# Optimization experiments

Measured on AMD Instinct MI355X. Metric: run time of the kernel, lower is better.

The kernel has to match this reference:

```python
import jax, jax.numpy as jnp
import numpy as np
from jax.scipy.special import logsumexp

VOCAB, NLABEL, NSTATE = 32000, 16, 64
BATCH, MAXLEN = 512, 512


def setup_inputs() -> dict:
    key = jax.random.key(0)
    k1, k2, k3, k4, k5 = jax.random.split(key, 5)
    sentences = jax.random.randint(k1, (BATCH, MAXLEN), 0, VOCAB)
    length = jax.random.randint(k2, (BATCH,), 1, MAXLEN + 1)  # valid lengths in [1, MAXLEN]
    # parameters, uniform(-0.5, 0.5) as in reset_parameter()
    emb = jax.random.uniform(k3, (VOCAB, NSTATE), minval=-0.5, maxval=0.5, dtype=jnp.float32)
    transition = jax.random.uniform(k4, (NSTATE, NSTATE), minval=-0.5, maxval=0.5, dtype=jnp.float32)
    output = jax.random.uniform(k5, (NLABEL, NSTATE), minval=-0.5, maxval=0.5, dtype=jnp.float32)
    return {"sentences": sentences, "length": length, "emb": emb,
            "transition": transition, "output": output}


def reference(sentences, length, emb, transition, output):
    batch = sentences.shape[0]
    # emission log-probs per timestep: [T, B, S]
    emission = jax.nn.log_softmax(emb[sentences.T], axis=-1)
    trans = jax.nn.log_softmax(transition, axis=-1)  # [S, S]

    def step(f, e):
        # log-space matrix-vector product: logsumexp over previous state
        nf = logsumexp(trans[None, :, :] + f[:, None, :], axis=-1) + e  # [B, S]
        return nf, nf

    f0 = emission[0]
    _, rest = jax.lax.scan(step, f0, emission[1:])
    forwards = jnp.concatenate([f0[None], rest], axis=0)  # [T, B, S]
    hidden = forwards[length - 1, jnp.arange(batch)]  # [B, S]
    out_log = jax.nn.log_softmax(output, axis=-1)  # [L, S]
    score = logsumexp(out_log[None, :, :] + hidden[:, None, :], axis=-1)  # [B, L]
    return score
```

## Files before the change

### kernel.cpp

```cpp
#include <hip/hip_runtime.h>
#include <stdint.h>

#define VOCAB  32000
#define NSTATE 64
#define NLABEL 16
#define BATCH  512
#define MAXLEN 512
#define CHUNK  64
#define NC     (MAXLEN / CHUNK)

#define LOG2E 1.44269504088896340736f
#define LN2_D 0.69314718055994530942

typedef float  f32x4  __attribute__((ext_vector_type(4)));
typedef short  bf16x8 __attribute__((ext_vector_type(8)));
typedef float  v2f    __attribute__((ext_vector_type(2)));

#if defined(__has_builtin) && __has_builtin(__builtin_amdgcn_exp2f)
#define EXP2(x) __builtin_amdgcn_exp2f(x)
#else
#define EXP2(x) exp2f(x)
#endif
#if defined(__has_builtin) && __has_builtin(__builtin_amdgcn_logf)
#define LOG2(x) __builtin_amdgcn_logf(x)
#else
#define LOG2(x) log2f(x)
#endif

__device__ __forceinline__ float wave_max64(float x) {
#pragma unroll
  for (int off = 32; off > 0; off >>= 1) x = fmaxf(x, __shfl_xor(x, off, 64));
  return x;
}
__device__ __forceinline__ float wave_sum64(float x) {
#pragma unroll
  for (int off = 32; off > 0; off >>= 1) x += __shfl_xor(x, off, 64);
  return x;
}
__device__ __forceinline__ float bcast0(float x) {
  return __uint_as_float(__builtin_amdgcn_readfirstlane(__float_as_uint(x)));
}
__device__ __forceinline__ double shfl_xor_d(double x, int off) {
  union { double d; int i[2]; } u;
  u.d = x;
  u.i[0] = __shfl_xor(u.i[0], off, 64);
  u.i[1] = __shfl_xor(u.i[1], off, 64);
  return u.d;
}
__device__ __forceinline__ unsigned short f2bf(float x) {
  uint32_t u = __float_as_uint(x);
  return (unsigned short)((u + 0x7FFFu + ((u >> 16) & 1u)) >> 16);
}
__device__ __forceinline__ float bf2f(unsigned short h) {
  return __uint_as_float(((uint32_t)h) << 16);
}
__device__ __forceinline__ int swz(int a) { return a ^ (((a >> 7) & 7) << 4); }

__global__ void prep_emb_k(const float* __restrict__ emb, float* __restrict__ emb2) {
  const int w = blockIdx.x * 4 + (threadIdx.x >> 6);
  const int s = threadIdx.x & 63;
  const float v = emb[w * NSTATE + s] * LOG2E;
  const float m = wave_max64(v);
  const float ss = wave_sum64(EXP2(v - m));
  emb2[w * NSTATE + s] = v - m - LOG2(ss);
}

__global__ void prep_mats_k(const float* __restrict__ trans, const float* __restrict__ outp,
                            float* __restrict__ W, float* __restrict__ out2) {
  const int r = blockIdx.x, s = threadIdx.x;
  if (r < NSTATE) {
    const float v = trans[r * NSTATE + s] * LOG2E;
    const float m = wave_max64(v);
    const float ss = wave_sum64(EXP2(v - m));
    W[r * NSTATE + s] = EXP2(v - m - LOG2(ss));
  } else {
    const int l = r - NSTATE;
    const float v = outp[l * NSTATE + s] * LOG2E;
    const float m = wave_max64(v);
    const float ss = wave_sum64(EXP2(v - m));
    out2[l * NSTATE + s] = v - m - LOG2(ss);
  }
}

__global__ void prep_wfrag_k(const float* __restrict__ W, bf16x8* __restrict__ Wb) {
  const int l = threadIdx.x;
  const int l15 = l & 15, lh = l >> 4;
#pragma unroll
  for (int mi = 0; mi < 4; ++mi)
#pragma unroll
    for (int ks = 0; ks < 2; ++ks) {
      bf16x8 v;
#pragma unroll
      for (int i = 0; i < 8; ++i)
        v[i] = (short)f2bf(W[(mi * 16 + l15) * 64 + ks * 32 + 8 * lh + i]);
      Wb[(mi * 2 + ks) * 64 + l] = v;
    }
}

__global__ void prep_musum2_k(const int* __restrict__ sents, const float* __restrict__ emb2,
                              const int* __restrict__ length, double* __restrict__ musum) {
  const int b = blockIdx.x;
  const int l = threadIdx.x;
  const int len = length[b];
  double acc = 0.0;
#pragma unroll
  for (int k = 0; k < 8; ++k) {
    const int t = k * 64 + l;
    const int id = sents[b * MAXLEN + t];
    const float e0 = emb2[id * NSTATE];
    if (t < len) acc += (double)e0;
  }
#pragma unroll
  for (int off = 32; off > 0; off >>= 1) acc += shfl_xor_d(acc, off);
  if (l == 0) musum[b] = acc;
}

__global__ __launch_bounds__(64, 2) void phaseA_k(
    const int* __restrict__ sents, const int* __restrict__ length,
    const float* __restrict__ emb2, const bf16x8* __restrict__ Wb,
    unsigned short* __restrict__ Mout, int* __restrict__ Mexp) {
  const int tid = blockIdx.x;
  const int b = tid >> 3;
  const int c = tid & 7;
  const int l = threadIdx.x;
  const int l15 = l & 15, lh = l >> 4;

  __shared__ __align__(16) unsigned short MT[4096];
  __shared__ __align__(16) float q_lds[NSTATE];
  __shared__ __align__(16) int ids[CHUNK];

  ids[l] = sents[b * MAXLEN + c * CHUNK + l];

  bf16x8 wf[4][2];
#pragma unroll
  for (int mi = 0; mi < 4; ++mi)
#pragma unroll
    for (int ks = 0; ks < 2; ++ks)
      wf[mi][ks] = Wb[(mi * 2 + ks) * 64 + l];

  {
    const int4 z{0, 0, 0, 0};
#pragma unroll
    for (int k = 0; k < 8; ++k)
      *reinterpret_cast<int4*>(reinterpret_cast<char*>(MT) + k * 1024 + l * 16) = z;
    const int dbyte = swz(128 * l + 2 * l);
    *reinterpret_cast<unsigned short*>(reinterpret_cast<char*>(MT) + dbyte) = 0x3F80u;
  }

  const int len = length[b];
  const int t0 = c * CHUNK;
  const int start = (c == 0) ? 1 : t0;
  const int end_ = ((len - 1) < (t0 + CHUNK - 1)) ? (len - 1) : (t0 + CHUNK - 1);
  const int K = end_ - start + 1;
  int MUc = 0;

  if (K > 0) {
    int idx = start - t0;
    int idc = ids[idx];
    float e_cur = emb2[idc * NSTATE + l];
    float rnorm = 1.0f;
    bool rn_pending = false;

    for (int j = 0; j < K; ++j) {
      const int idxn = (j + 1 < K) ? (idx + 1) : idx;
      const int idn = ids[idxn];
      const float e_nxt = emb2[idn * NSTATE + l];

      const float se = bcast0(e_cur);
      q_lds[l] = EXP2(e_cur - se);

      float samp = 0.f;
#pragma unroll
      for (int pass = 0; pass < 2; ++pass) {
        bf16x8 mf[2][2];
#pragma unroll
        for (int ks = 0; ks < 2; ++ks)
#pragma unroll
          for (int nn = 0; nn < 2; ++nn) {
            const int n = (pass * 2 + nn) * 16 + l15;
            const int byte = swz(128 * n + 64 * ks + 16 * lh);
            mf[ks][nn] = *reinterpret_cast<const bf16x8*>(
                reinterpret_cast<const char*>(MT) + byte);
          }
#pragma unroll
        for (int mi = 0; mi < 4; ++mi) {
          f32x4 qf = *reinterpret_cast<const f32x4*>(q_lds + mi * 16 + 4 * lh);
          if (rn_pending) qf *= rnorm;
#pragma unroll
          for (int nn = 0; nn < 2; ++nn) {
            f32x4 acc{0.f, 0.f, 0.f, 0.f};
            acc = __builtin_amdgcn_mfma_f32_16x16x32_bf16(wf[mi][0], mf[0][nn], acc, 0, 0, 0);
            acc = __builtin_amdgcn_mfma_f32_16x16x32_bf16(wf[mi][1], mf[1][nn], acc, 0, 0, 0);
            acc *= qf;
            if (pass == 0 && nn == 0 && mi == 0) samp = acc.x;
            const uint32_t lo = (uint32_t)f2bf(acc.x) | ((uint32_t)f2bf(acc.y) << 16);
            const uint32_t hi = (uint32_t)f2bf(acc.z) | ((uint32_t)f2bf(acc.w) << 16);
            const int n = (pass * 2 + nn) * 16 + l15;
            const int wbyte = swz(128 * n + 2 * (mi * 16 + 4 * lh));
            *reinterpret_cast<uint2*>(reinterpret_cast<char*>(MT) + wbyte) = uint2{lo, hi};
          }
        }
      }
      rn_pending = false;
      if (((j & 7) == 7) && (j + 1 < K)) {
        const uint32_t u = __builtin_amdgcn_readfirstlane(__float_as_uint(samp));
        const int ex = (int)((u >> 23) & 255u) - 127;
        rnorm = __uint_as_float((uint32_t)(127 - ex) << 23);
        rn_pending = true;
        MUc += ex;
      }
      e_cur = e_nxt;
      idx = idxn;
    }
  }

  unsigned short* dst = Mout + (size_t)tid * 4096;
#pragma unroll
  for (int k = 0; k < 8; ++k) {
    const int4 v = *reinterpret_cast<const int4*>(
        reinterpret_cast<const char*>(MT) + k * 1024 + l * 16);
    *reinterpret_cast<int4*>(reinterpret_cast<char*>(dst) + k * 1024 + l * 16) = v;
  }
  if (l == 0) Mexp[tid] = MUc;
}

__global__ __launch_bounds__(64) void phaseB_k(
    const int* __restrict__ sents, const int* __restrict__ length,
    const float* __restrict__ emb2, const float* __restrict__ out2,
    const unsigned short* __restrict__ Mout, const int* __restrict__ Mexp,
    const double* __restrict__ musum, float* __restrict__ score) {
  const int b = blockIdx.x;
  const int l = threadIdx.x;
  const int len = length[b];

  const int id0 = sents[b * MAXLEN];
  const float e0 = emb2[id0 * NSTATE + l];
  const float se0 = bcast0(e0);
  float p = EXP2(e0 - se0);
  int MUi = 0;

  for (int c = 0; c < NC && c * CHUNK < len; ++c) {
    const unsigned short* M = Mout + ((size_t)(b * NC + c)) * 4096;
    float acc = 0.f;
#pragma unroll 8
    for (int n = 0; n < 64; ++n) {
      const float pn = __shfl(p, n, 64);
      const int byte = swz(128 * n + 2 * l);
      const unsigned short h = *reinterpret_cast<const unsigned short*>(
          reinterpret_cast<const char*>(M) + byte);
      acc = fmaf(bf2f(h), pn, acc);
    }
    p = acc;
    MUi += Mexp[b * NC + c];
    const uint32_t u = __builtin_amdgcn_readfirstlane(__float_as_uint(p));
    const int ex = (int)((u >> 23) & 255u) - 127;
    p *= __uint_as_float((uint32_t)(127 - ex) << 23);
    MUi += ex;
  }

  const float f = LOG2(p);
  const double base = musum[b] + (double)MUi;
  for (int ll = 0; ll < NLABEL; ++ll) {
    const float y = out2[ll * NSTATE + l] + f;
    const float m = wave_max64(y);
    const float ssum = wave_sum64(EXP2(y - m));
    if (l == 0)
      score[b * NLABEL + ll] = (float)((base + (double)m + (double)LOG2(ssum)) * LN2_D);
  }
}

__global__ __launch_bounds__(64, 1) void iohmm_fwd_fb(
    const int* __restrict__ sents, const int* __restrict__ length,
    const float* __restrict__ emb, const float* __restrict__ trans,
    const float* __restrict__ outp, float* __restrict__ score) {
  const int b = blockIdx.x;
  const int s = threadIdx.x;
  __shared__ __align__(16) float p_lds[2][NSTATE];
  v2f w2[NSTATE / 2];
  {
    float wr[NSTATE];
#pragma unroll
    for (int j = 0; j < 16; ++j) {
      const float4 q = *reinterpret_cast<const float4*>(trans + s * NSTATE + 4 * j);
      wr[4 * j + 0] = q.x * LOG2E; wr[4 * j + 1] = q.y * LOG2E;
      wr[4 * j + 2] = q.z * LOG2E; wr[4 * j + 3] = q.w * LOG2E;
    }
    float m = -1e30f;
#pragma unroll
    for (int j = 0; j < NSTATE; ++j) m = fmaxf(m, wr[j]);
    float ss = 0.f;
#pragma unroll
    for (int j = 0; j < NSTATE; ++j) ss += EXP2(wr[j] - m);
    const float d = m + LOG2(ss);
#pragma unroll
    for (int j = 0; j < NSTATE / 2; ++j)
      w2[j] = v2f{EXP2(wr[2 * j] - d), EXP2(wr[2 * j + 1] - d)};
  }
  const int len = length[b];
  auto EMIT = [&](int t) -> float {
    const int tc = t < MAXLEN ? t : MAXLEN - 1;
    return emb[sents[b * MAXLEN + tc] * NSTATE + s] * LOG2E;
  };
  float e0 = EMIT(0);
  {
    const float dm = wave_max64(e0);
    const float dsum = wave_sum64(EXP2(e0 - dm));
    e0 = e0 - dm - LOG2(dsum);
  }
  const float se0 = bcast0(e0);
  float p = EXP2(e0 - se0);
  double MU = (double)se0;
  int MUi = 0;
  for (int t = 1; t < len; ++t) {
    float* pb = p_lds[t & 1];
    pb[s] = p;
    __builtin_amdgcn_sched_barrier(0);
    const float eR = EMIT(t);
    const float4* pb4 = reinterpret_cast<const float4*>(pb);
    v2f A0{0.f, 0.f}, A1 = A0, A2 = A0, A3 = A0;
#pragma unroll
    for (int j = 0; j < 8; ++j) {
      const float4 qa = pb4[2 * j + 0];
      const float4 qb = pb4[2 * j + 1];
      A0 = __builtin_elementwise_fma(w2[4 * j + 0], v2f{qa.x, qa.y}, A0);
      A1 = __builtin_elementwise_fma(w2[4 * j + 1], v2f{qa.z, qa.w}, A1);
      A2 = __builtin_elementwise_fma(w2[4 * j + 2], v2f{qb.x, qb.y}, A2);
      A3 = __builtin_elementwise_fma(w2[4 * j + 3], v2f{qb.z, qb.w}, A3);
    }
    const v2f S0 = A0 + A2, S1 = A1 + A3;
    const v2f U = S0 + S1;
    const float sum = U.x + U.y;
    const float dm = wave_max64(eR);
    const float dsum = wave_sum64(EXP2(eR - dm));
    const float e = eR - dm - LOG2(dsum);
    const float se = bcast0(e);
    p = sum * EXP2(e - se);
    if ((t & 15) == 0) {
      const uint32_t u = __builtin_amdgcn_readfirstlane(__float_as_uint(p));
      const int ex = (int)((u >> 23) & 255u) - 127;
      p *= __uint_as_float((uint32_t)(127 - ex) << 23);
      MUi += ex;
    }
    MU += (double)se;
  }
  const float f = LOG2(p);
  const double MUt = MU + (double)MUi;
  for (int ll = 0; ll < NLABEL; ++ll) {
    const float v = outp[ll * NSTATE + s] * LOG2E;
    const float lm = wave_max64(v);
    const float lsum = wave_sum64(EXP2(v - lm));
    const float y = v - lm - LOG2(lsum) + f;
    const float m = wave_max64(y);
    const float ssum = wave_sum64(EXP2(y - m));
    if (s == 0)
      score[b * NLABEL + ll] = (float)((MUt + (double)m + (double)LOG2(ssum)) * LN2_D);
  }
}

extern "C" void kernel_launch(void* const* d_in, const int* in_sizes, int n_in,
                              void* d_out, int out_size, void* d_ws, size_t ws_size,
                              hipStream_t stream) {
  const int* sents = (const int*)d_in[0];
  const int* length = (const int*)d_in[1];
  const float* emb = (const float*)d_in[2];
  const float* trans = (const float*)d_in[3];
  const float* outp = (const float*)d_in[4];
  float* score = (float*)d_out;

  const size_t emb2_off = 0;
  const size_t emb2_sz = (size_t)VOCAB * NSTATE * sizeof(float);
  const size_t W_off = emb2_off + emb2_sz;
  const size_t W_sz = NSTATE * NSTATE * sizeof(float);
  const size_t out2_off = W_off + W_sz;
  const size_t out2_sz = NLABEL * NSTATE * sizeof(float);
  const size_t Wb_off = out2_off + out2_sz;
  const size_t Wb_sz = 8 * 64 * 16;
  const size_t musum_off = Wb_off + Wb_sz;
  const size_t musum_sz = BATCH * sizeof(double);
  const size_t Mexp_off = musum_off + musum_sz;
  const size_t Mexp_sz = (size_t)BATCH * NC * sizeof(int);
  const size_t Mout_off = Mexp_off + Mexp_sz;
  const size_t Mout_sz = (size_t)BATCH * NC * 4096 * sizeof(unsigned short);
  const size_t need = Mout_off + Mout_sz;

  if (ws_size >= need) {
    float* emb2 = (float*)((char*)d_ws + emb2_off);
    float* W = (float*)((char*)d_ws + W_off);
    float* out2 = (float*)((char*)d_ws + out2_off);
    bf16x8* Wb = (bf16x8*)((char*)d_ws + Wb_off);
    double* musum = (double*)((char*)d_ws + musum_off);
    int* Mexp = (int*)((char*)d_ws + Mexp_off);
    unsigned short* Mout = (unsigned short*)((char*)d_ws + Mout_off);

    prep_emb_k<<<VOCAB / 4, 256, 0, stream>>>(emb, emb2);
    prep_mats_k<<<NSTATE + NLABEL, 64, 0, stream>>>(trans, outp, W, out2);
    prep_wfrag_k<<<1, 64, 0, stream>>>(W, Wb);
    prep_musum2_k<<<BATCH, 64, 0, stream>>>(sents, emb2, length, musum);
    phaseA_k<<<BATCH * NC, 64, 0, stream>>>(sents, length, emb2, Wb, Mout, Mexp);
    phaseB_k<<<BATCH, 64, 0, stream>>>(sents, length, emb2, out2, Mout, Mexp, musum, score);
  } else {
    iohmm_fwd_fb<<<BATCH, 64, 0, stream>>>(sents, length, emb, trans, outp, score);
  }
}
```

Before: 304.4 us.

## Fold prep kernels into phase kernels and pack four chunk waves per block

```diff
diff --git a/kernel.cpp b/kernel.cpp
--- a/kernel.cpp
+++ b/kernel.cpp
@@ -1,4 +1,5 @@
 #include <hip/hip_runtime.h>
+#include <hip/hip_bf16.h>
 #include <stdint.h>
 
 #define VOCAB  32000
@@ -47,9 +48,12 @@
   u.i[1] = __shfl_xor(u.i[1], off, 64);
   return u.d;
 }
-__device__ __forceinline__ unsigned short f2bf(float x) {
-  uint32_t u = __float_as_uint(x);
-  return (unsigned short)((u + 0x7FFFu + ((u >> 16) & 1u)) >> 16);
+__device__ __forceinline__ short bfs(float x) {
+  __hip_bfloat16 h = __float2bfloat16(x);
+  return *reinterpret_cast<short*>(&h);
+}
+__device__ __forceinline__ uint32_t pkbf(float lo, float hi) {
+  return (uint32_t)(unsigned short)bfs(lo) | ((uint32_t)(unsigned short)bfs(hi) << 16);
 }
 __device__ __forceinline__ float bf2f(unsigned short h) {
   return __uint_as_float(((uint32_t)h) << 16);
@@ -82,69 +86,42 @@
   }
 }
 
-__global__ void prep_wfrag_k(const float* __restrict__ W, bf16x8* __restrict__ Wb) {
-  const int l = threadIdx.x;
-  const int l15 = l & 15, lh = l >> 4;
-#pragma unroll
-  for (int mi = 0; mi < 4; ++mi)
-#pragma unroll
-    for (int ks = 0; ks < 2; ++ks) {
-      bf16x8 v;
-#pragma unroll
-      for (int i = 0; i < 8; ++i)
-        v[i] = (short)f2bf(W[(mi * 16 + l15) * 64 + ks * 32 + 8 * lh + i]);
-      Wb[(mi * 2 + ks) * 64 + l] = v;
-    }
-}
-
-__global__ void prep_musum2_k(const int* __restrict__ sents, const float* __restrict__ emb2,
-                              const int* __restrict__ length, double* __restrict__ musum) {
-  const int b = blockIdx.x;
-  const int l = threadIdx.x;
-  const int len = length[b];
-  double acc = 0.0;
-#pragma unroll
-  for (int k = 0; k < 8; ++k) {
-    const int t = k * 64 + l;
-    const int id = sents[b * MAXLEN + t];
-    const float e0 = emb2[id * NSTATE];
-    if (t < len) acc += (double)e0;
-  }
-#pragma unroll
-  for (int off = 32; off > 0; off >>= 1) acc += shfl_xor_d(acc, off);
-  if (l == 0) musum[b] = acc;
-}
-
-__global__ __launch_bounds__(64, 2) void phaseA_k(
+__global__ __launch_bounds__(256, 4) void phaseA_k(
     const int* __restrict__ sents, const int* __restrict__ length,
-    const float* __restrict__ emb2, const bf16x8* __restrict__ Wb,
+    const float* __restrict__ emb2, const float* __restrict__ W,
     unsigned short* __restrict__ Mout, int* __restrict__ Mexp) {
-  const int tid = blockIdx.x;
+  const int wid = threadIdx.x >> 6;
+  const int l = threadIdx.x & 63;
+  const int tid = blockIdx.x * 4 + wid;
   const int b = tid >> 3;
   const int c = tid & 7;
-  const int l = threadIdx.x;
   const int l15 = l & 15, lh = l >> 4;
 
-  __shared__ __align__(16) unsigned short MT[4096];
-  __shared__ __align__(16) float q_lds[NSTATE];
-  __shared__ __align__(16) int ids[CHUNK];
-
-  ids[l] = sents[b * MAXLEN + c * CHUNK + l];
+  __shared__ __align__(16) unsigned short MTall[4][4096];
+  char* MTc = reinterpret_cast<char*>(MTall[wid]);
+
+  const int myid = sents[b * MAXLEN + c * CHUNK + l];
 
   bf16x8 wf[4][2];
 #pragma unroll
   for (int mi = 0; mi < 4; ++mi)
 #pragma unroll
-    for (int ks = 0; ks < 2; ++ks)
-      wf[mi][ks] = Wb[(mi * 2 + ks) * 64 + l];
+    for (int ks = 0; ks < 2; ++ks) {
+      const float* wp = W + (mi * 16 + l15) * 64 + ks * 32 + 8 * lh;
+      const float4 a = *reinterpret_cast<const float4*>(wp);
+      const float4 d = *reinterpret_cast<const float4*>(wp + 4);
+      bf16x8 v;
+      v[0] = bfs(a.x); v[1] = bfs(a.y); v[2] = bfs(a.z); v[3] = bfs(a.w);
+      v[4] = bfs(d.x); v[5] = bfs(d.y); v[6] = bfs(d.z); v[7] = bfs(d.w);
+      wf[mi][ks] = v;
+    }
 
   {
     const int4 z{0, 0, 0, 0};
 #pragma unroll
     for (int k = 0; k < 8; ++k)
-      *reinterpret_cast<int4*>(reinterpret_cast<char*>(MT) + k * 1024 + l * 16) = z;
-    const int dbyte = swz(128 * l + 2 * l);
-    *reinterpret_cast<unsigned short*>(reinterpret_cast<char*>(MT) + dbyte) = 0x3F80u;
+      *reinterpret_cast<int4*>(MTc + k * 1024 + l * 16) = z;
+    *reinterpret_cast<unsigned short*>(MTc + swz(130 * l)) = 0x3F80u;
   }
 
   const int len = length[b];
@@ -155,19 +132,28 @@
   int MUc = 0;
 
   if (K > 0) {
-    int idx = start - t0;
-    int idc = ids[idx];
-    float e_cur = emb2[idc * NSTATE + l];
+    const int lastj = end_ - t0;
+    const int j0 = start - t0;
+    float eA = emb2[(size_t)__shfl(myid, j0, 64) * 64 + l];
+    const int j1 = (j0 + 1 <= lastj) ? j0 + 1 : lastj;
+    float eB = emb2[(size_t)__shfl(myid, j1, 64) * 64 + l];
     float rnorm = 1.0f;
-    bool rn_pending = false;
+    bool rnp = false;
 
     for (int j = 0; j < K; ++j) {
-      const int idxn = (j + 1 < K) ? (idx + 1) : idx;
-      const int idn = ids[idxn];
-      const float e_nxt = emb2[idn * NSTATE + l];
-
-      const float se = bcast0(e_cur);
-      q_lds[l] = EXP2(e_cur - se);
+      int jn = j0 + j + 2; jn = (jn <= lastj) ? jn : lastj;
+      const float eC = emb2[(size_t)__shfl(myid, jn, 64) * 64 + l];
+
+      const float se = bcast0(eA);
+      float qv = EXP2(eA - se);
+      if (rnp) qv *= rnorm;
+
+      float qsc[4][4];
+#pragma unroll
+      for (int mi = 0; mi < 4; ++mi)
+#pragma unroll
+        for (int r = 0; r < 4; ++r)
+          qsc[mi][r] = __shfl(qv, mi * 16 + 4 * lh + r, 64);
 
       float samp = 0.f;
 #pragma unroll
@@ -178,47 +164,43 @@
 #pragma unroll
           for (int nn = 0; nn < 2; ++nn) {
             const int n = (pass * 2 + nn) * 16 + l15;
-            const int byte = swz(128 * n + 64 * ks + 16 * lh);
             mf[ks][nn] = *reinterpret_cast<const bf16x8*>(
-                reinterpret_cast<const char*>(MT) + byte);
+                MTc + swz(128 * n + 64 * ks + 16 * lh));
           }
 #pragma unroll
         for (int mi = 0; mi < 4; ++mi) {
-          f32x4 qf = *reinterpret_cast<const f32x4*>(q_lds + mi * 16 + 4 * lh);
-          if (rn_pending) qf *= rnorm;
 #pragma unroll
           for (int nn = 0; nn < 2; ++nn) {
             f32x4 acc{0.f, 0.f, 0.f, 0.f};
             acc = __builtin_amdgcn_mfma_f32_16x16x32_bf16(wf[mi][0], mf[0][nn], acc, 0, 0, 0);
             acc = __builtin_amdgcn_mfma_f32_16x16x32_bf16(wf[mi][1], mf[1][nn], acc, 0, 0, 0);
-            acc *= qf;
+            acc.x *= qsc[mi][0]; acc.y *= qsc[mi][1];
+            acc.z *= qsc[mi][2]; acc.w *= qsc[mi][3];
             if (pass == 0 && nn == 0 && mi == 0) samp = acc.x;
-            const uint32_t lo = (uint32_t)f2bf(acc.x) | ((uint32_t)f2bf(acc.y) << 16);
-            const uint32_t hi = (uint32_t)f2bf(acc.z) | ((uint32_t)f2bf(acc.w) << 16);
+            const uint32_t lo = pkbf(acc.x, acc.y);
+            const uint32_t hi = pkbf(acc.z, acc.w);
             const int n = (pass * 2 + nn) * 16 + l15;
-            const int wbyte = swz(128 * n + 2 * (mi * 16 + 4 * lh));
-            *reinterpret_cast<uint2*>(reinterpret_cast<char*>(MT) + wbyte) = uint2{lo, hi};
+            *reinterpret_cast<uint2*>(MTc + swz(128 * n + 32 * mi + 8 * lh)) =
+                uint2{lo, hi};
           }
         }
       }
-      rn_pending = false;
+      rnp = false;
       if (((j & 7) == 7) && (j + 1 < K)) {
         const uint32_t u = __builtin_amdgcn_readfirstlane(__float_as_uint(samp));
         const int ex = (int)((u >> 23) & 255u) - 127;
         rnorm = __uint_as_float((uint32_t)(127 - ex) << 23);
-        rn_pending = true;
+        rnp = true;
         MUc += ex;
       }
-      e_cur = e_nxt;
-      idx = idxn;
+      eA = eB; eB = eC;
     }
   }
 
   unsigned short* dst = Mout + (size_t)tid * 4096;
 #pragma unroll
   for (int k = 0; k < 8; ++k) {
-    const int4 v = *reinterpret_cast<const int4*>(
-        reinterpret_cast<const char*>(MT) + k * 1024 + l * 16);
+    const int4 v = *reinterpret_cast<const int4*>(MTc + k * 1024 + l * 16);
     *reinterpret_cast<int4*>(reinterpret_cast<char*>(dst) + k * 1024 + l * 16) = v;
   }
   if (l == 0) Mexp[tid] = MUc;
@@ -228,13 +210,22 @@
     const int* __restrict__ sents, const int* __restrict__ length,
     const float* __restrict__ emb2, const float* __restrict__ out2,
     const unsigned short* __restrict__ Mout, const int* __restrict__ Mexp,
-    const double* __restrict__ musum, float* __restrict__ score) {
+    float* __restrict__ score) {
   const int b = blockIdx.x;
   const int l = threadIdx.x;
   const int len = length[b];
 
+  double ms = 0.0;
+#pragma unroll
+  for (int k = 0; k < 8; ++k) {
+    const int t = k * 64 + l;
+    const int id = sents[b * MAXLEN + t];
+    const float e0 = emb2[(size_t)id * NSTATE];
+    if (t < len) ms += (double)e0;
+  }
+
   const int id0 = sents[b * MAXLEN];
-  const float e0 = emb2[id0 * NSTATE + l];
+  const float e0 = emb2[(size_t)id0 * NSTATE + l];
   const float se0 = bcast0(e0);
   float p = EXP2(e0 - se0);
   int MUi = 0;
@@ -245,9 +236,8 @@
 #pragma unroll 8
     for (int n = 0; n < 64; ++n) {
       const float pn = __shfl(p, n, 64);
-      const int byte = swz(128 * n + 2 * l);
       const unsigned short h = *reinterpret_cast<const unsigned short*>(
-          reinterpret_cast<const char*>(M) + byte);
+          reinterpret_cast<const char*>(M) + swz(128 * n + 2 * l));
       acc = fmaf(bf2f(h), pn, acc);
     }
     p = acc;
@@ -258,8 +248,11 @@
     MUi += ex;
   }
 
+#pragma unroll
+  for (int off = 32; off > 0; off >>= 1) ms += shfl_xor_d(ms, off);
+
   const float f = LOG2(p);
-  const double base = musum[b] + (double)MUi;
+  const double base = ms + (double)MUi;
   for (int ll = 0; ll < NLABEL; ++ll) {
     const float y = out2[ll * NSTATE + l] + f;
     const float m = wave_max64(y);
@@ -373,11 +366,7 @@
   const size_t W_sz = NSTATE * NSTATE * sizeof(float);
   const size_t out2_off = W_off + W_sz;
   const size_t out2_sz = NLABEL * NSTATE * sizeof(float);
-  const size_t Wb_off = out2_off + out2_sz;
-  const size_t Wb_sz = 8 * 64 * 16;
-  const size_t musum_off = Wb_off + Wb_sz;
-  const size_t musum_sz = BATCH * sizeof(double);
-  const size_t Mexp_off = musum_off + musum_sz;
+  const size_t Mexp_off = out2_off + out2_sz;
   const size_t Mexp_sz = (size_t)BATCH * NC * sizeof(int);
   const size_t Mout_off = Mexp_off + Mexp_sz;
   const size_t Mout_sz = (size_t)BATCH * NC * 4096 * sizeof(unsigned short);
@@ -387,17 +376,13 @@
     float* emb2 = (float*)((char*)d_ws + emb2_off);
     float* W = (float*)((char*)d_ws + W_off);
     float* out2 = (float*)((char*)d_ws + out2_off);
-    bf16x8* Wb = (bf16x8*)((char*)d_ws + Wb_off);
-    double* musum = (double*)((char*)d_ws + musum_off);
     int* Mexp = (int*)((char*)d_ws + Mexp_off);
     unsigned short* Mout = (unsigned short*)((char*)d_ws + Mout_off);
 
     prep_emb_k<<<VOCAB / 4, 256, 0, stream>>>(emb, emb2);
     prep_mats_k<<<NSTATE + NLABEL, 64, 0, stream>>>(trans, outp, W, out2);
-    prep_wfrag_k<<<1, 64, 0, stream>>>(W, Wb);
-    prep_musum2_k<<<BATCH, 64, 0, stream>>>(sents, emb2, length, musum);
-    phaseA_k<<<BATCH * NC, 64, 0, stream>>>(sents, length, emb2, Wb, Mout, Mexp);
-    phaseB_k<<<BATCH, 64, 0, stream>>>(sents, length, emb2, out2, Mout, Mexp, musum, score);
+    phaseA_k<<<BATCH * NC / 4, 256, 0, stream>>>(sents, length, emb2, W, Mout, Mexp);
+    phaseB_k<<<BATCH, 64, 0, stream>>>(sents, length, emb2, out2, Mout, Mexp, score);
   } else {
     iohmm_fwd_fb<<<BATCH, 64, 0, stream>>>(sents, length, emb, trans, outp, score);
   }
```

New measurement: 283.0 us. 1.08x faster.
